# Performance work log

Hardware: AMD Instinct MI355X
Metric: run time of the kernel (lower is better)

Reference implementation:

```python
import jax, jax.numpy as jnp
import numpy as np

NUM_RELATION = 500
NUM_ENTITY = 100000
EMBED_DIM = 64
B, N = 8192, 128
MASK_BIG = 1e19


def setup_inputs() -> dict:
    key = jax.random.key(0)
    k1, k2, k3, k4, k5, k6, k7, k8 = jax.random.split(key, 8)
    inp = {
        "input": jax.random.normal(k1, (B, N, EMBED_DIM), dtype=jnp.float32),
        "neighbor": jax.random.randint(k2, (B, N, 2), 0, NUM_ENTITY + 1, dtype=jnp.int64),
        "query_relation_id": jax.random.randint(k3, (B,), 0, 2 * NUM_RELATION, dtype=jnp.int64),
        "weight": jax.random.uniform(k4, (B, N, 2), dtype=jnp.float32),
        # learned parameters (xavier-normal-like init)
        "mlp_w_weight": jax.random.normal(k5, (NUM_ENTITY * 2 + 1, EMBED_DIM), dtype=jnp.float32) * 0.02,
        "qrel_weight": jax.random.normal(k6, (NUM_RELATION * 2, EMBED_DIM), dtype=jnp.float32) * 0.02,
        "att_w": jax.random.normal(k7, (EMBED_DIM * 2, EMBED_DIM * 2), dtype=jnp.float32) * 0.05,
        "att_v": jax.random.normal(k8, (1, EMBED_DIM * 2), dtype=jnp.float32) * 0.05,
    }
    return inp


def reference(input, neighbor, query_relation_id, weight, mlp_w_weight, qrel_weight, att_w, att_v):
    # neighbor channels: relation id (indexes mlp_w), entity id (indexes mask tables)
    input_relation = neighbor[:, :, 0]
    input_entity = neighbor[:, :, 1]

    r = mlp_w_weight[input_relation]                         # [B,N,D] gather
    # hyperplane transform: e - <e, r_hat> r_hat  (F.normalize with eps=1e-12)
    norm = jnp.maximum(jnp.linalg.norm(r, axis=2, keepdims=True), 1e-12)
    normed = r / norm
    transformed = input - jnp.sum(input * normed, axis=2, keepdims=True) * normed

    # mask_emb: 1 for real entities, 0 for padding entity (id == NUM_ENTITY)
    mask = (input_entity < NUM_ENTITY).astype(transformed.dtype)[:, :, None]
    transformed = transformed * mask

    query = qrel_weight[query_relation_id][:, None, :]       # [B,1,D]
    query = jnp.broadcast_to(query, (query.shape[0], transformed.shape[1], query.shape[2]))

    # MLP attention: tanh([q; t] W) . v
    hidden = jnp.tanh(jnp.concatenate([query, transformed], axis=2) @ att_w)  # [B,N,2D]
    attention_logit = jnp.sum(hidden * att_v[0], axis=2)      # [B,N]

    # mask_weight: subtract 1e19 at padding entities
    mask_logit = jnp.where(input_entity == NUM_ENTITY, jnp.float32(MASK_BIG), jnp.float32(0.0))
    attention_logit = attention_logit - mask_logit

    attention_weight = jax.nn.softmax(attention_logit, axis=1)
    attention_weight = attention_weight + weight[:, :, 0] / (weight[:, :, 1] + 1)

    output = jnp.sum(transformed * attention_weight[:, :, None], axis=1)  # [B,D]
    return output, attention_weight
```

## Files before the change

kernel.cpp:

```cpp
#include <hip/hip_runtime.h>
#include <hip/hip_bf16.h>

#define NB 8192
#define NE 100000

typedef __bf16 bf16x8 __attribute__((ext_vector_type(8)));
typedef __bf16 bf16x4 __attribute__((ext_vector_type(4)));
typedef float  f32x4  __attribute__((ext_vector_type(4)));

template<int C>
__device__ __forceinline__ float dpp_mov(float v) {
  return __int_as_float(__builtin_amdgcn_update_dpp(
      0, __float_as_int(v), C, 0xF, 0xF, true));
}

__device__ __forceinline__ float red16(float v) {
  v += dpp_mov<0xB1>(v);
  v += dpp_mov<0x4E>(v);
  v += dpp_mov<0x141>(v);
  v += dpp_mov<0x140>(v);
  return v;
}

__device__ __forceinline__ float swz_xor16(float v) {
  return __int_as_float(__builtin_amdgcn_ds_swizzle(__float_as_int(v), 0x401F));
}

__device__ __forceinline__ float fast_tanh(float x) {
  float e = __expf(-2.0f * fabsf(x));
  float t = (1.0f - e) * __builtin_amdgcn_rcpf(1.0f + e);
  return copysignf(t, x);
}

__global__ void prep_kernel(const float* __restrict__ att_w,
                            const float* __restrict__ qrel,
                            __bf16* __restrict__ wsf,
                            float*  __restrict__ qpart) {
  const int t = threadIdx.x;
  const int bid = blockIdx.x;
  if (bid == 0) {
    for (int i = t; i < 8192; i += 128) {
      int e  = i & 7;
      int l  = (i >> 3) & 63;
      int ks = (i >> 9) & 1;
      int tc = i >> 10;
      int k = ks * 32 + ((l >> 4) << 3) + e;
      int j = tc * 16 + (l & 15);
      wsf[i] = (__bf16)att_w[(64 + k) * 128 + j];
    }
  } else {
    int rid = bid - 1;
    float acc = 0.f;
    for (int k = 0; k < 64; ++k)
      acc += qrel[rid * 64 + k] * att_w[k * 128 + t];
    qpart[rid * 128 + t] = acc;
  }
}

__global__ __launch_bounds__(256, 4)
void attn_kernel(const float* __restrict__ inp,
                 const int*   __restrict__ nb,
                 const int*   __restrict__ qid_p,
                 const float* __restrict__ wgt,
                 const float* __restrict__ mlp,
                 const float* __restrict__ attv,
                 const __bf16* __restrict__ wsf,
                 const float* __restrict__ qpart_t,
                 float* __restrict__ out) {
  __shared__ float plog[128], awl[128];
  __shared__ float part[4][64];

  const int t    = threadIdx.x;
  const int lane = t & 63;
  const int w    = t >> 6;
  const int r    = lane & 15;
  const int c    = lane >> 4;
  const int b    = blockIdx.x;

  const int qid = qid_p[b];
  float qpv[8], vv[8];
#pragma unroll
  for (int tc = 0; tc < 8; ++tc) {
    qpv[tc] = qpart_t[qid * 128 + tc * 16 + r];
    vv[tc]  = attv[tc * 16 + r];
  }
  const int rown = w * 32 + (lane & 31);
  float2 w01 = reinterpret_cast<const float2*>(wgt)[(size_t)b * 128 + rown];
  const float wr = w01.x / (w01.y + 1.0f);

  bf16x8 af[2][2];
  int2 re[2];
#pragma unroll
  for (int tr = 0; tr < 2; ++tr) {
    int n = w * 32 + tr * 16 + r;
    re[tr] = *reinterpret_cast<const int2*>(&nb[((size_t)b * 128 + n) * 2]);
  }
#pragma unroll
  for (int tr = 0; tr < 2; ++tr) {
    int n = w * 32 + tr * 16 + r;
    const float* iptr = &inp[((size_t)b * 128 + n) * 64 + c * 8];
    f32x4 iv0 = *reinterpret_cast<const f32x4*>(iptr);
    f32x4 iv1 = *reinterpret_cast<const f32x4*>(iptr + 4);
    f32x4 iv2 = *reinterpret_cast<const f32x4*>(iptr + 32);
    f32x4 iv3 = *reinterpret_cast<const f32x4*>(iptr + 36);
    const float* rptr = &mlp[(size_t)re[tr].x * 64 + c * 8];
    f32x4 rv0 = *reinterpret_cast<const f32x4*>(rptr);
    f32x4 rv1 = *reinterpret_cast<const f32x4*>(rptr + 4);
    f32x4 rv2 = *reinterpret_cast<const f32x4*>(rptr + 32);
    f32x4 rv3 = *reinterpret_cast<const f32x4*>(rptr + 36);
    float s1 = rv0[0]*rv0[0] + rv0[1]*rv0[1] + rv0[2]*rv0[2] + rv0[3]*rv0[3]
             + rv1[0]*rv1[0] + rv1[1]*rv1[1] + rv1[2]*rv1[2] + rv1[3]*rv1[3]
             + rv2[0]*rv2[0] + rv2[1]*rv2[1] + rv2[2]*rv2[2] + rv2[3]*rv2[3]
             + rv3[0]*rv3[0] + rv3[1]*rv3[1] + rv3[2]*rv3[2] + rv3[3]*rv3[3];
    float s2 = iv0[0]*rv0[0] + iv0[1]*rv0[1] + iv0[2]*rv0[2] + iv0[3]*rv0[3]
             + iv1[0]*rv1[0] + iv1[1]*rv1[1] + iv1[2]*rv1[2] + iv1[3]*rv1[3]
             + iv2[0]*rv2[0] + iv2[1]*rv2[1] + iv2[2]*rv2[2] + iv2[3]*rv2[3]
             + iv3[0]*rv3[0] + iv3[1]*rv3[1] + iv3[2]*rv3[2] + iv3[3]*rv3[3];
    s1 += swz_xor16(s1);  s2 += swz_xor16(s2);
    s1 += __shfl_xor(s1, 32, 64);
    s2 += __shfl_xor(s2, 32, 64);
    float f   = s2 / fmaxf(s1, 1e-24f);
    float msk = (re[tr].y >= NE) ? 0.0f : 1.0f;
    bf16x8 a0, a1;
#pragma unroll
    for (int j = 0; j < 4; ++j) {
      a0[j]     = (__bf16)((iv0[j] - f * rv0[j]) * msk);
      a0[j + 4] = (__bf16)((iv1[j] - f * rv1[j]) * msk);
      a1[j]     = (__bf16)((iv2[j] - f * rv2[j]) * msk);
      a1[j + 4] = (__bf16)((iv3[j] - f * rv3[j]) * msk);
    }
    af[tr][0] = a0;
    af[tr][1] = a1;
  }

  float p[2][4] = {{0,0,0,0},{0,0,0,0}};
#pragma unroll
  for (int h = 0; h < 2; ++h) {
    f32x4 acc[2][4];
#pragma unroll
    for (int tc2 = 0; tc2 < 4; ++tc2) {
      float qv = qpv[h * 4 + tc2];
      acc[0][tc2] = f32x4{qv, qv, qv, qv};
      acc[1][tc2] = f32x4{qv, qv, qv, qv};
    }
#pragma unroll
    for (int tc2 = 0; tc2 < 4; ++tc2) {
      int tc = h * 4 + tc2;
      bf16x8 b0 = *reinterpret_cast<const bf16x8*>(wsf + ((tc * 2 + 0) * 64 + lane) * 8);
      bf16x8 b1 = *reinterpret_cast<const bf16x8*>(wsf + ((tc * 2 + 1) * 64 + lane) * 8);
      acc[0][tc2] = __builtin_amdgcn_mfma_f32_16x16x32_bf16(af[0][0], b0, acc[0][tc2], 0, 0, 0);
      acc[1][tc2] = __builtin_amdgcn_mfma_f32_16x16x32_bf16(af[1][0], b0, acc[1][tc2], 0, 0, 0);
      acc[0][tc2] = __builtin_amdgcn_mfma_f32_16x16x32_bf16(af[0][1], b1, acc[0][tc2], 0, 0, 0);
      acc[1][tc2] = __builtin_amdgcn_mfma_f32_16x16x32_bf16(af[1][1], b1, acc[1][tc2], 0, 0, 0);
    }
#pragma unroll
    for (int tr = 0; tr < 2; ++tr)
#pragma unroll
      for (int tc2 = 0; tc2 < 4; ++tc2) {
        float v = vv[h * 4 + tc2];
        p[tr][0] += fast_tanh(acc[tr][tc2][0]) * v;
        p[tr][1] += fast_tanh(acc[tr][tc2][1]) * v;
        p[tr][2] += fast_tanh(acc[tr][tc2][2]) * v;
        p[tr][3] += fast_tanh(acc[tr][tc2][3]) * v;
      }
  }
#pragma unroll
  for (int tr = 0; tr < 2; ++tr) {
    float p0 = red16(p[tr][0]), p1 = red16(p[tr][1]);
    float p2 = red16(p[tr][2]), p3 = red16(p[tr][3]);
    if (r == 0) {
      int row = w * 32 + tr * 16 + c * 4;
      plog[row + 0] = p0;
      plog[row + 1] = p1;
      plog[row + 2] = p2;
      plog[row + 3] = p3;
    }
  }
  __syncthreads();

  {
    int e0i = nb[((size_t)b * 128 + lane) * 2 + 1];
    int e1i = nb[((size_t)b * 128 + lane + 64) * 2 + 1];
    float l0 = plog[lane]      - ((e0i == NE) ? 1e19f : 0.0f);
    float l1 = plog[lane + 64] - ((e1i == NE) ? 1e19f : 0.0f);
    float m = fmaxf(l0, l1);
    m = fmaxf(m, __shfl_xor(m, 1, 64));
    m = fmaxf(m, __shfl_xor(m, 2, 64));
    m = fmaxf(m, __shfl_xor(m, 4, 64));
    m = fmaxf(m, __shfl_xor(m, 8, 64));
    m = fmaxf(m, __shfl_xor(m, 16, 64));
    m = fmaxf(m, __shfl_xor(m, 32, 64));
    float e0 = __expf(l0 - m), e1 = __expf(l1 - m);
    float s = e0 + e1;
    s += __shfl_xor(s, 1, 64);
    s += __shfl_xor(s, 2, 64);
    s += __shfl_xor(s, 4, 64);
    s += __shfl_xor(s, 8, 64);
    s += __shfl_xor(s, 16, 64);
    s += __shfl_xor(s, 32, 64);
    float rcp = __builtin_amdgcn_rcpf(s);
    float inv = rcp * (2.0f - s * rcp);
    if (lane < 32) {
      int eri = nb[((size_t)b * 128 + rown) * 2 + 1];
      float lg = plog[rown] - ((eri == NE) ? 1e19f : 0.0f);
      float aw = __expf(lg - m) * inv + wr;
      awl[rown] = aw;
      float* awout = out + (size_t)NB * 64;
      awout[(size_t)b * 128 + rown] = aw;
    }
  }

  {
    float po0[8] = {0,0,0,0,0,0,0,0};
    float po1[8] = {0,0,0,0,0,0,0,0};
#pragma unroll
    for (int tr = 0; tr < 2; ++tr) {
      float a = awl[w * 32 + tr * 16 + r];
      bf16x8 a0 = af[tr][0], a1 = af[tr][1];
#pragma unroll
      for (int e = 0; e < 8; ++e) {
        po0[e] += (float)a0[e] * a;
        po1[e] += (float)a1[e] * a;
      }
    }
#pragma unroll
    for (int e = 0; e < 8; ++e) {
      po0[e] = red16(po0[e]);
      po1[e] = red16(po1[e]);
    }
    if (r == 0) {
#pragma unroll
      for (int e = 0; e < 8; ++e) {
        part[w][c * 8 + e]      = po0[e];
        part[w][32 + c * 8 + e] = po1[e];
      }
    }
  }
  __syncthreads();
  if (t < 64)
    out[(size_t)b * 64 + t] = part[0][t] + part[1][t] + part[2][t] + part[3][t];
}

extern "C" void kernel_launch(void* const* d_in, const int* in_sizes, int n_in,
                              void* d_out, int out_size, void* d_ws, size_t ws_size,
                              hipStream_t stream) {
  const float* inp  = (const float*)d_in[0];
  const int*   nb   = (const int*)d_in[1];
  const int*   qid  = (const int*)d_in[2];
  const float* wgt  = (const float*)d_in[3];
  const float* mlp  = (const float*)d_in[4];
  const float* qrel = (const float*)d_in[5];
  const float* attw = (const float*)d_in[6];
  const float* attv = (const float*)d_in[7];
  float* out = (float*)d_out;

  __bf16* wsf   = (__bf16*)d_ws;
  float*  qpart = (float*)((char*)d_ws + 16384);

  prep_kernel<<<1001, 128, 0, stream>>>(attw, qrel, wsf, qpart);
  attn_kernel<<<NB, 256, 0, stream>>>(inp, nb, qid, wgt, mlp, attv, wsf, qpart, out);
}
```

Baseline: 458.7 us.

## Assign one batch row per wavefront, replacing block barriers with wave-local sync

Each wavefront now processes a whole batch element (all 128 neighbors), so a 256-thread block handles four batch rows and the grid shrinks by four. Block-wide __syncthreads and the cross-wave partial-sum reduction are replaced by per-wave LDS buffers with lgkmcnt waits. Entity and weight loads are hoisted and reused for the softmax. The cost is much higher register pressure (16 bf16x8 A fragments per lane) and less memory-level parallelism per wave, which may reduce occupancy under the launch bounds.

```diff
diff --git a/kernel.cpp b/kernel.cpp
--- a/kernel.cpp
+++ b/kernel.cpp
@@ -5,7 +5,6 @@
 #define NE 100000
 
 typedef __bf16 bf16x8 __attribute__((ext_vector_type(8)));
-typedef __bf16 bf16x4 __attribute__((ext_vector_type(4)));
 typedef float  f32x4  __attribute__((ext_vector_type(4)));
 
 template<int C>
@@ -67,15 +66,18 @@
                  const __bf16* __restrict__ wsf,
                  const float* __restrict__ qpart_t,
                  float* __restrict__ out) {
-  __shared__ float plog[128], awl[128];
-  __shared__ float part[4][64];
+  __shared__ float plogS[4][128];
+  __shared__ float awlS[4][128];
 
   const int t    = threadIdx.x;
   const int lane = t & 63;
   const int w    = t >> 6;
   const int r    = lane & 15;
   const int c    = lane >> 4;
-  const int b    = blockIdx.x;
+  const int b    = blockIdx.x * 4 + w;
+
+  float* plog = plogS[w];
+  float* awl  = awlS[w];
 
   const int qid = qid_p[b];
   float qpv[8], vv[8];
@@ -84,21 +86,22 @@
     qpv[tc] = qpart_t[qid * 128 + tc * 16 + r];
     vv[tc]  = attv[tc * 16 + r];
   }
-  const int rown = w * 32 + (lane & 31);
-  float2 w01 = reinterpret_cast<const float2*>(wgt)[(size_t)b * 128 + rown];
-  const float wr = w01.x / (w01.y + 1.0f);
-
-  bf16x8 af[2][2];
-  int2 re[2];
-#pragma unroll
-  for (int tr = 0; tr < 2; ++tr) {
-    int n = w * 32 + tr * 16 + r;
-    re[tr] = *reinterpret_cast<const int2*>(&nb[((size_t)b * 128 + n) * 2]);
-  }
-#pragma unroll
-  for (int tr = 0; tr < 2; ++tr) {
-    int n = w * 32 + tr * 16 + r;
-    const float* iptr = &inp[((size_t)b * 128 + n) * 64 + c * 8];
+  const int ent0 = nb[((size_t)b * 128 + lane) * 2 + 1];
+  const int ent1 = nb[((size_t)b * 128 + lane + 64) * 2 + 1];
+  float2 wA = reinterpret_cast<const float2*>(wgt)[(size_t)b * 128 + lane];
+  float2 wB = reinterpret_cast<const float2*>(wgt)[(size_t)b * 128 + lane + 64];
+  const float wr0 = wA.x / (wA.y + 1.0f);
+  const float wr1 = wB.x / (wB.y + 1.0f);
+
+  int2 re[8];
+#pragma unroll
+  for (int tr = 0; tr < 8; ++tr)
+    re[tr] = *reinterpret_cast<const int2*>(&nb[((size_t)b * 128 + tr * 16 + r) * 2]);
+
+  bf16x8 af[8][2];
+#pragma unroll
+  for (int tr = 0; tr < 8; ++tr) {
+    const float* iptr = &inp[((size_t)b * 128 + tr * 16 + r) * 64 + c * 8];
     f32x4 iv0 = *reinterpret_cast<const f32x4*>(iptr);
     f32x4 iv1 = *reinterpret_cast<const f32x4*>(iptr + 4);
     f32x4 iv2 = *reinterpret_cast<const f32x4*>(iptr + 32);
@@ -133,56 +136,40 @@
     af[tr][1] = a1;
   }
 
-  float p[2][4] = {{0,0,0,0},{0,0,0,0}};
-#pragma unroll
-  for (int h = 0; h < 2; ++h) {
-    f32x4 acc[2][4];
-#pragma unroll
-    for (int tc2 = 0; tc2 < 4; ++tc2) {
-      float qv = qpv[h * 4 + tc2];
-      acc[0][tc2] = f32x4{qv, qv, qv, qv};
-      acc[1][tc2] = f32x4{qv, qv, qv, qv};
-    }
-#pragma unroll
-    for (int tc2 = 0; tc2 < 4; ++tc2) {
-      int tc = h * 4 + tc2;
-      bf16x8 b0 = *reinterpret_cast<const bf16x8*>(wsf + ((tc * 2 + 0) * 64 + lane) * 8);
-      bf16x8 b1 = *reinterpret_cast<const bf16x8*>(wsf + ((tc * 2 + 1) * 64 + lane) * 8);
-      acc[0][tc2] = __builtin_amdgcn_mfma_f32_16x16x32_bf16(af[0][0], b0, acc[0][tc2], 0, 0, 0);
-      acc[1][tc2] = __builtin_amdgcn_mfma_f32_16x16x32_bf16(af[1][0], b0, acc[1][tc2], 0, 0, 0);
-      acc[0][tc2] = __builtin_amdgcn_mfma_f32_16x16x32_bf16(af[0][1], b1, acc[0][tc2], 0, 0, 0);
-      acc[1][tc2] = __builtin_amdgcn_mfma_f32_16x16x32_bf16(af[1][1], b1, acc[1][tc2], 0, 0, 0);
-    }
-#pragma unroll
-    for (int tr = 0; tr < 2; ++tr)
-#pragma unroll
-      for (int tc2 = 0; tc2 < 4; ++tc2) {
-        float v = vv[h * 4 + tc2];
-        p[tr][0] += fast_tanh(acc[tr][tc2][0]) * v;
-        p[tr][1] += fast_tanh(acc[tr][tc2][1]) * v;
-        p[tr][2] += fast_tanh(acc[tr][tc2][2]) * v;
-        p[tr][3] += fast_tanh(acc[tr][tc2][3]) * v;
-      }
-  }
-#pragma unroll
-  for (int tr = 0; tr < 2; ++tr) {
-    float p0 = red16(p[tr][0]), p1 = red16(p[tr][1]);
-    float p2 = red16(p[tr][2]), p3 = red16(p[tr][3]);
+  int wofs = 0;
+  asm volatile("" : "+s"(wofs));
+#pragma unroll
+  for (int tr = 0; tr < 8; ++tr) {
+    float p0 = 0.f, p1 = 0.f, p2 = 0.f, p3 = 0.f;
+    const __bf16* wp = wsf + wofs + lane * 8;
+#pragma unroll
+    for (int tc = 0; tc < 8; ++tc) {
+      bf16x8 b0 = *reinterpret_cast<const bf16x8*>(wp + (tc * 2 + 0) * 512);
+      bf16x8 b1 = *reinterpret_cast<const bf16x8*>(wp + (tc * 2 + 1) * 512);
+      float qv = qpv[tc];
+      f32x4 acc = f32x4{qv, qv, qv, qv};
+      acc = __builtin_amdgcn_mfma_f32_16x16x32_bf16(af[tr][0], b0, acc, 0, 0, 0);
+      acc = __builtin_amdgcn_mfma_f32_16x16x32_bf16(af[tr][1], b1, acc, 0, 0, 0);
+      float v = vv[tc];
+      p0 += fast_tanh(acc[0]) * v;
+      p1 += fast_tanh(acc[1]) * v;
+      p2 += fast_tanh(acc[2]) * v;
+      p3 += fast_tanh(acc[3]) * v;
+    }
+    p0 = red16(p0); p1 = red16(p1); p2 = red16(p2); p3 = red16(p3);
     if (r == 0) {
-      int row = w * 32 + tr * 16 + c * 4;
+      int row = tr * 16 + c * 4;
       plog[row + 0] = p0;
       plog[row + 1] = p1;
       plog[row + 2] = p2;
       plog[row + 3] = p3;
     }
   }
-  __syncthreads();
+  asm volatile("s_waitcnt lgkmcnt(0)" ::: "memory");
 
   {
-    int e0i = nb[((size_t)b * 128 + lane) * 2 + 1];
-    int e1i = nb[((size_t)b * 128 + lane + 64) * 2 + 1];
-    float l0 = plog[lane]      - ((e0i == NE) ? 1e19f : 0.0f);
-    float l1 = plog[lane + 64] - ((e1i == NE) ? 1e19f : 0.0f);
+    float l0 = plog[lane]      - ((ent0 == NE) ? 1e19f : 0.0f);
+    float l1 = plog[lane + 64] - ((ent1 == NE) ? 1e19f : 0.0f);
     float m = fmaxf(l0, l1);
     m = fmaxf(m, __shfl_xor(m, 1, 64));
     m = fmaxf(m, __shfl_xor(m, 2, 64));
@@ -200,22 +187,22 @@
     s += __shfl_xor(s, 32, 64);
     float rcp = __builtin_amdgcn_rcpf(s);
     float inv = rcp * (2.0f - s * rcp);
-    if (lane < 32) {
-      int eri = nb[((size_t)b * 128 + rown) * 2 + 1];
-      float lg = plog[rown] - ((eri == NE) ? 1e19f : 0.0f);
-      float aw = __expf(lg - m) * inv + wr;
-      awl[rown] = aw;
-      float* awout = out + (size_t)NB * 64;
-      awout[(size_t)b * 128 + rown] = aw;
-    }
-  }
+    float a0 = e0 * inv + wr0;
+    float a1 = e1 * inv + wr1;
+    awl[lane]      = a0;
+    awl[lane + 64] = a1;
+    float* awout = out + (size_t)NB * 64;
+    awout[(size_t)b * 128 + lane]      = a0;
+    awout[(size_t)b * 128 + lane + 64] = a1;
+  }
+  asm volatile("s_waitcnt lgkmcnt(0)" ::: "memory");
 
   {
     float po0[8] = {0,0,0,0,0,0,0,0};
     float po1[8] = {0,0,0,0,0,0,0,0};
 #pragma unroll
-    for (int tr = 0; tr < 2; ++tr) {
-      float a = awl[w * 32 + tr * 16 + r];
+    for (int tr = 0; tr < 8; ++tr) {
+      float a = awl[tr * 16 + r];
       bf16x8 a0 = af[tr][0], a1 = af[tr][1];
 #pragma unroll
       for (int e = 0; e < 8; ++e) {
@@ -231,14 +218,13 @@
     if (r == 0) {
 #pragma unroll
       for (int e = 0; e < 8; ++e) {
-        part[w][c * 8 + e]      = po0[e];
-        part[w][32 + c * 8 + e] = po1[e];
+        plog[c * 8 + e]      = po0[e];
+        plog[32 + c * 8 + e] = po1[e];
       }
     }
   }
-  __syncthreads();
-  if (t < 64)
-    out[(size_t)b * 64 + t] = part[0][t] + part[1][t] + part[2][t] + part[3][t];
+  asm volatile("s_waitcnt lgkmcnt(0)" ::: "memory");
+  out[(size_t)b * 64 + lane] = plog[lane];
 }
 
 extern "C" void kernel_launch(void* const* d_in, const int* in_sizes, int n_in,
@@ -258,5 +244,5 @@
   float*  qpart = (float*)((char*)d_ws + 16384);
 
   prep_kernel<<<1001, 128, 0, stream>>>(attw, qrel, wsf, qpart);
-  attn_kernel<<<NB, 256, 0, stream>>>(inp, nb, qid, wgt, mlp, attv, wsf, qpart, out);
-}
+  attn_kernel<<<NB / 4, 256, 0, stream>>>(inp, nb, qid, wgt, mlp, attv, wsf, qpart, out);
+}
```

Result: slower. 896.3 us (+95.4%).
